# Optimization experiments

Measured on AMD Instinct MI355X. Metric: run time of the kernel, lower is better.

Reference implementation:

```python
import jax, jax.numpy as jnp
import numpy as np

N, N1, N2, K = 65536, 16384, 8192, 16
INDIM, HID, OUT = 64, 32, 128


def _knn_np(pos, q, k, chunk=1024):
    # brute-force chunked KNN (indices into pos) for setup only
    out = []
    for s in range(0, q.shape[0], chunk):
        d = ((q[s:s + chunk, None, :] - pos[None, :, :]) ** 2).sum(-1)
        out.append(np.argpartition(d, k, axis=1)[:, :k])
    return np.concatenate(out, 0)


def setup_inputs() -> dict:
    key = jax.random.key(0)
    ks = jax.random.split(key, 12)
    x = jax.random.normal(ks[0], (N, INDIM), jnp.float32)
    pos = jax.random.uniform(ks[1], (N, 3), jnp.float32)

    pos_np = np.asarray(pos)
    rng = np.random.default_rng(0)
    idx1 = np.sort(rng.choice(N, N1, replace=False))            # RandomSampler(ratio1)
    nn1 = _knn_np(pos_np, pos_np[idx1], K)                      # [N1, K] into full cloud
    src1, dst1 = nn1.reshape(-1), np.repeat(np.arange(N1), K)
    pos1 = pos_np[idx1]
    idx2 = np.sort(rng.choice(N1, N2, replace=False))           # RandomSampler(ratio2)
    nn2 = _knn_np(pos1, pos1[idx2], K)                          # [N2, K] into level-1 cloud
    src2, dst2 = nn2.reshape(-1), np.repeat(np.arange(N2), K)

    def lin(k, i, o):
        return jax.random.normal(k, (i, o), jnp.float32) / float(np.sqrt(i))

    return dict(
        x=x, pos=pos,
        W_down=lin(ks[2], INDIM, HID), b_down=jnp.zeros((HID,), jnp.float32),
        W_pp1=lin(ks[3], 10, 32), b_pp1=jnp.zeros((32,), jnp.float32),
        W_att1=lin(ks[4], 64, 64), b_att1=jnp.zeros((64,), jnp.float32),
        W_g1=lin(ks[5], 64, 64), b_g1=jnp.zeros((64,), jnp.float32),
        W_pp2=lin(ks[6], 10, 64), b_pp2=jnp.zeros((64,), jnp.float32),
        W_att2=lin(ks[7], 128, 128), b_att2=jnp.zeros((128,), jnp.float32),
        W_g2=lin(ks[8], 128, 128), b_g2=jnp.zeros((128,), jnp.float32),
        W_up=lin(ks[9], 128, OUT), b_up=jnp.zeros((OUT,), jnp.float32),
        W_sc=lin(ks[10], INDIM, OUT), b_sc=jnp.zeros((OUT,), jnp.float32),
        idx1=jnp.asarray(idx1, jnp.int32), idx2=jnp.asarray(idx2, jnp.int32),
        src1=jnp.asarray(src1, jnp.int32), dst1=jnp.asarray(dst1, jnp.int32),
        src2=jnp.asarray(src2, jnp.int32), dst2=jnp.asarray(dst2, jnp.int32),
    )


def _mlp(h, W, b):
    return jax.nn.relu(h @ W + b)


def _randla_conv(x, pos_all, pos_q, src, dst, Wpp, bpp, Watt, batt, Wg, bg, n_out):
    # RandlaKernel.message + add-aggregate + update (bipartite: targets = sampled points)
    pos_i, pos_j = pos_q[dst], pos_all[src]                     # [E,3]
    vij = pos_i - pos_j
    dij = jnp.sqrt((vij * vij).sum(-1, keepdims=True))          # [E,1]
    rel = jnp.concatenate([pos_i, pos_j, vij, dij], axis=1)     # [E,10]
    rij = _mlp(rel, Wpp, bpp)                                   # point_pos_nn
    fij = jnp.concatenate([x[src], rij], axis=1)                # [E, c+d]
    s = jax.nn.softmax(_mlp(fij, Watt, batt), axis=-1)          # softmax over feature dim (as in source)
    agg = jax.ops.segment_sum(s * fij, dst, num_segments=n_out) # aggr='add'
    return _mlp(agg, Wg, bg)                                    # global_nn


def reference(x, pos, W_down, b_down, W_pp1, b_pp1, W_att1, b_att1, W_g1, b_g1,
              W_pp2, b_pp2, W_att2, b_att2, W_g2, b_g2, W_up, b_up, W_sc, b_sc,
              idx1, idx2, src1, dst1, src2, dst2):
    h = _mlp(x, W_down, b_down)                                 # features_downsample (indim -> outdim//4)
    pos1 = pos[idx1]
    h = _randla_conv(h, pos, pos1, src1, dst1, W_pp1, b_pp1, W_att1, b_att1, W_g1, b_g1, N1)
    pos2 = pos1[idx2]
    h = _randla_conv(h, pos1, pos2, src2, dst2, W_pp2, b_pp2, W_att2, b_att2, W_g2, b_g2, N2)
    h = _mlp(h, W_up, b_up)                                     # features_upsample
    sc = _mlp(x[idx1][idx2], W_sc, b_sc)                        # shortcut resized, idx = idx1[idx2]
    return jax.nn.relu(h + sc)
```

## Files before the change

### kernel.cpp

```cpp
#include <hip/hip_runtime.h>

#define N_FULL 65536
#define NN1    16384
#define NN2    8192

typedef __attribute__((ext_vector_type(8))) short bf16x8;
typedef __attribute__((ext_vector_type(4))) float f32x4;
typedef unsigned short ushortT;

#define MFMA16(acc, a, b) acc = __builtin_amdgcn_mfma_f32_16x16x32_bf16(a, b, acc, 0, 0, 0)

static __device__ __forceinline__ ushortT f2bf(float f) {
    union { float f; unsigned u; } v; v.f = f;
    unsigned r = v.u + 0x7FFFu + ((v.u >> 16) & 1u);
    return (ushortT)(r >> 16);
}
static __device__ __forceinline__ unsigned pack2(float a, float b) {
    return (unsigned)f2bf(a) | ((unsigned)f2bf(b) << 16);
}
static __device__ __forceinline__ float bfu2f(ushortT h) {
    union { unsigned u; float f; } v; v.u = (unsigned)h << 16; return v.f;
}

#define WS_WDT   0
#define WS_WAT1  2304
#define WS_WGT1  6912
#define WS_WAT2  11520
#define WS_WGT2  28928
#define WS_WUPT  46336
#define WS_WSCT  63744
#define WS_H0    73728
#define WS_H1    (WS_H0 + 65536u*32u)
#define WS_AGG2  (WS_H1 + 16384u*64u)

static __device__ __forceinline__ void tpose(
    const float* __restrict__ src, ushortT* __restrict__ dst,
    int K, int N, int STR, int gid, int gs)
{
    for (int i = gid; i < K * N; i += gs) {
        const int n = i / K, k = i - n * K;
        dst[n * STR + k] = f2bf(src[(size_t)k * N + n]);
    }
}

__global__ __launch_bounds__(256) void k_prep(
    const float* __restrict__ Wd, const float* __restrict__ Wa1,
    const float* __restrict__ Wg1, const float* __restrict__ Wa2,
    const float* __restrict__ Wg2, const float* __restrict__ Wup,
    const float* __restrict__ Wsc, ushortT* __restrict__ wsw)
{
    const int gid = blockIdx.x * 256 + threadIdx.x, gs = gridDim.x * 256;
    tpose(Wd,  wsw + WS_WDT,  64, 32, 72,  gid, gs);
    tpose(Wa1, wsw + WS_WAT1, 64, 64, 72,  gid, gs);
    tpose(Wg1, wsw + WS_WGT1, 64, 64, 72,  gid, gs);
    tpose(Wa2, wsw + WS_WAT2, 128, 128, 136, gid, gs);
    tpose(Wg2, wsw + WS_WGT2, 128, 128, 136, gid, gs);
    tpose(Wup, wsw + WS_WUPT, 128, 128, 136, gid, gs);
    tpose(Wsc, wsw + WS_WSCT, 64, 128, 72, gid, gs);
}

__global__ __launch_bounds__(256) void k_down(
    const float* __restrict__ x, const ushortT* __restrict__ wsw,
    const float* __restrict__ bd, ushortT* __restrict__ h0w)
{
    __shared__ __align__(16) ushortT Al[128 * 72];
    __shared__ __align__(16) ushortT Bl[32 * 72];
    const int t = threadIdx.x;
    const int rowBase = blockIdx.x * 128;

    {
        const int r = t >> 1, c0 = (t & 1) * 32;
        unsigned* dst = (unsigned*)Al + r * 36 + (c0 >> 1);
        const float* src = &x[(size_t)(rowBase + r) * 64 + c0];
#pragma unroll
        for (int j = 0; j < 32; j += 4) {
            const float4 v = *reinterpret_cast<const float4*>(src + j);
            dst[(j >> 1) + 0] = pack2(v.x, v.y);
            dst[(j >> 1) + 1] = pack2(v.z, v.w);
        }
        const uint4* wsrc = (const uint4*)(wsw + WS_WDT);
        uint4* bl4 = (uint4*)Bl;
        for (int i = t; i < 288; i += 256) bl4[i] = wsrc[i];
    }
    __syncthreads();

    const int lane = t & 63, w = t >> 6, quad = lane >> 4, c16 = lane & 15;
    f32x4 acc[2][2];
#pragma unroll
    for (int mt = 0; mt < 2; ++mt)
#pragma unroll
        for (int nt = 0; nt < 2; ++nt)
#pragma unroll
            for (int r = 0; r < 4; ++r) acc[mt][nt][r] = 0.f;
#pragma unroll
    for (int ks = 0; ks < 2; ++ks) {
        bf16x8 a[2], b[2];
#pragma unroll
        for (int mt = 0; mt < 2; ++mt)
            a[mt] = *(const bf16x8*)&Al[(w * 32 + mt * 16 + c16) * 72 + ks * 32 + quad * 8];
#pragma unroll
        for (int nt = 0; nt < 2; ++nt)
            b[nt] = *(const bf16x8*)&Bl[(nt * 16 + c16) * 72 + ks * 32 + quad * 8];
#pragma unroll
        for (int mt = 0; mt < 2; ++mt)
#pragma unroll
            for (int nt = 0; nt < 2; ++nt) MFMA16(acc[mt][nt], a[mt], b[nt]);
    }
#pragma unroll
    for (int nt = 0; nt < 2; ++nt) {
        const int col = nt * 16 + c16;
        const float bias = bd[col];
#pragma unroll
        for (int mt = 0; mt < 2; ++mt)
#pragma unroll
            for (int r = 0; r < 4; ++r) {
                const int row = rowBase + w * 32 + mt * 16 + quad * 4 + r;
                h0w[(size_t)row * 32 + col] = f2bf(fmaxf(acc[mt][nt][r] + bias, 0.f));
            }
    }
}

__global__ __launch_bounds__(256) void k_conv1(
    const ushortT* __restrict__ h0w, const float* __restrict__ pos,
    const int* __restrict__ idx1, const int* __restrict__ src1,
    const float* __restrict__ Wpp, const float* __restrict__ bpp,
    const ushortT* __restrict__ wsw, const float* __restrict__ batt,
    const float* __restrict__ bg, ushortT* __restrict__ h1w)
{
    __shared__ __align__(16) ushortT Fl[128 * 72];
    __shared__ __align__(16) ushortT Wl[64 * 72];
    __shared__ __align__(16) ushortT Gl[64 * 72];
    __shared__ __align__(16) ushortT A2ls[16 * 72];
    __shared__ float Pl[352];
    const int t = threadIdx.x;
    const int d0 = blockIdx.x * 8;

    {
        const uint4* wa = (const uint4*)(wsw + WS_WAT1);
        const uint4* wg = (const uint4*)(wsw + WS_WGT1);
        uint4* wl4 = (uint4*)Wl;
        uint4* gl4 = (uint4*)Gl;
        for (int i = t; i < 576; i += 256) { wl4[i] = wa[i]; gl4[i] = wg[i]; }
        for (int i = t; i < 352; i += 256) Pl[i] = (i < 320) ? Wpp[i] : bpp[i - 320];
        for (int i = t; i < 288; i += 256) ((unsigned*)A2ls)[288 + i] = 0;
    }

    {
        const int e = t >> 1, half = t & 1;
        const int g = e >> 4;
        const int s = src1[(d0 + g) * 16 + (e & 15)];
        const uint4* srcp = (const uint4*)((const unsigned*)h0w + (size_t)s * 16 + half * 8);
        uint4* dstp = (uint4*)((unsigned*)Fl + e * 36 + half * 8);
        dstp[0] = srcp[0];
        dstp[1] = srcp[1];

        const int pin = idx1[d0 + g];
        const float pix = pos[pin * 3 + 0], piy = pos[pin * 3 + 1], piz = pos[pin * 3 + 2];
        const float pjx = pos[s * 3 + 0],  pjy = pos[s * 3 + 1],  pjz = pos[s * 3 + 2];
        const float vx = pix - pjx, vy = piy - pjy, vz = piz - pjz;
        const float dij = sqrtf(vx * vx + vy * vy + vz * vz);
        const float rel[10] = {pix, piy, piz, pjx, pjy, pjz, vx, vy, vz, dij};
        __syncthreads();
        const int c0 = half * 16;
#pragma unroll
        for (int c = 0; c < 16; c += 2) {
            float a0 = Pl[320 + c0 + c], a1 = Pl[320 + c0 + c + 1];
#pragma unroll
            for (int i = 0; i < 10; ++i) {
                a0 += rel[i] * Pl[i * 32 + c0 + c];
                a1 += rel[i] * Pl[i * 32 + c0 + c + 1];
            }
            ((unsigned*)Fl)[(e * 72 + 32 + c0 + c) >> 1] = pack2(fmaxf(a0, 0.f), fmaxf(a1, 0.f));
        }
    }
    __syncthreads();

    const int lane = t & 63, w = t >> 6, quad = lane >> 4, c16 = lane & 15;
    f32x4 acc[2][4];
#pragma unroll
    for (int mt = 0; mt < 2; ++mt)
#pragma unroll
        for (int nt = 0; nt < 4; ++nt)
#pragma unroll
            for (int r = 0; r < 4; ++r) acc[mt][nt][r] = 0.f;
#pragma unroll
    for (int ks = 0; ks < 2; ++ks) {
        bf16x8 a[2], b[4];
#pragma unroll
        for (int mt = 0; mt < 2; ++mt)
            a[mt] = *(const bf16x8*)&Fl[(w * 32 + mt * 16 + c16) * 72 + ks * 32 + quad * 8];
#pragma unroll
        for (int nt = 0; nt < 4; ++nt)
            b[nt] = *(const bf16x8*)&Wl[(nt * 16 + c16) * 72 + ks * 32 + quad * 8];
#pragma unroll
        for (int mt = 0; mt < 2; ++mt)
#pragma unroll
            for (int nt = 0; nt < 4; ++nt) MFMA16(acc[mt][nt], a[mt], b[nt]);
    }
    float bcol[4];
#pragma unroll
    for (int nt = 0; nt < 4; ++nt) bcol[nt] = batt[nt * 16 + c16];

#pragma unroll
    for (int mt = 0; mt < 2; ++mt) {
#pragma unroll
        for (int nt = 0; nt < 4; ++nt)
#pragma unroll
            for (int r = 0; r < 4; ++r)
                acc[mt][nt][r] = fmaxf(acc[mt][nt][r] + bcol[nt], 0.f);
        float rs[4];
#pragma unroll
        for (int r = 0; r < 4; ++r) {
            float mx = acc[mt][0][r];
#pragma unroll
            for (int nt = 1; nt < 4; ++nt) mx = fmaxf(mx, acc[mt][nt][r]);
            mx = fmaxf(mx, __shfl_xor(mx, 1));
            mx = fmaxf(mx, __shfl_xor(mx, 2));
            mx = fmaxf(mx, __shfl_xor(mx, 4));
            mx = fmaxf(mx, __shfl_xor(mx, 8));
            float sm = 0.f;
#pragma unroll
            for (int nt = 0; nt < 4; ++nt) {
                acc[mt][nt][r] = __expf(acc[mt][nt][r] - mx);
                sm += acc[mt][nt][r];
            }
            sm += __shfl_xor(sm, 1);
            sm += __shfl_xor(sm, 2);
            sm += __shfl_xor(sm, 4);
            sm += __shfl_xor(sm, 8);
            rs[r] = 1.f / sm;
        }
#pragma unroll
        for (int nt = 0; nt < 4; ++nt) {
            float v = 0.f;
#pragma unroll
            for (int r = 0; r < 4; ++r) {
                const float fv = bfu2f(Fl[(w * 32 + mt * 16 + quad * 4 + r) * 72 + nt * 16 + c16]);
                v += acc[mt][nt][r] * rs[r] * fv;
            }
            v += __shfl_xor(v, 16);
            v += __shfl_xor(v, 32);
            if (lane < 16)
                A2ls[(w * 2 + mt) * 72 + nt * 16 + c16] = f2bf(v);
        }
    }
    __syncthreads();

    {
        f32x4 acc2 = {0.f, 0.f, 0.f, 0.f};
#pragma unroll
        for (int ks = 0; ks < 2; ++ks) {
            const bf16x8 a = *(const bf16x8*)&A2ls[c16 * 72 + ks * 32 + quad * 8];
            const bf16x8 b = *(const bf16x8*)&Gl[(w * 16 + c16) * 72 + ks * 32 + quad * 8];
            MFMA16(acc2, a, b);
        }
        const int col = w * 16 + c16;
        const float bias = bg[col];
        if (quad < 2) {
#pragma unroll
            for (int r = 0; r < 4; ++r) {
                const int row = quad * 4 + r;
                h1w[(size_t)(d0 + row) * 64 + col] = f2bf(fmaxf(acc2[r] + bias, 0.f));
            }
        }
    }
}

__global__ __launch_bounds__(256) void k_conv2(
    const ushortT* __restrict__ h1w, const float* __restrict__ pos,
    const int* __restrict__ idx1, const int* __restrict__ idx2,
    const int* __restrict__ src2,
    const float* __restrict__ Wpp, const float* __restrict__ bpp,
    const ushortT* __restrict__ wsw, const float* __restrict__ batt,
    ushortT* __restrict__ agg2w)
{
    __shared__ __align__(16) ushortT Fl[128 * 136];
    __shared__ __align__(16) ushortT Wl[128 * 136];
    __shared__ float Pl[704];
    const int t = threadIdx.x;
    const int d0 = blockIdx.x * 8;

    {
        const uint4* wsrc = (const uint4*)(wsw + WS_WAT2);
        uint4* wl4 = (uint4*)Wl;
        for (int i = t; i < 2176; i += 256) wl4[i] = wsrc[i];
        for (int i = t; i < 704; i += 256) Pl[i] = (i < 640) ? Wpp[i] : bpp[i - 640];
    }

    {
        const int e = t >> 1, half = t & 1;
        const int g = e >> 4;
        const int s = src2[(d0 + g) * 16 + (e & 15)];
        const uint4* srcp = (const uint4*)((const unsigned*)h1w + (size_t)s * 32 + half * 16);
        uint4* dstp = (uint4*)((unsigned*)Fl + e * 68 + half * 16);
#pragma unroll
        for (int j = 0; j < 4; ++j) dstp[j] = srcp[j];

        const int pin = idx1[idx2[d0 + g]];
        const int sn = idx1[s];
        const float pix = pos[pin * 3 + 0], piy = pos[pin * 3 + 1], piz = pos[pin * 3 + 2];
        const float pjx = pos[sn * 3 + 0],  pjy = pos[sn * 3 + 1],  pjz = pos[sn * 3 + 2];
        const float vx = pix - pjx, vy = piy - pjy, vz = piz - pjz;
        const float dij = sqrtf(vx * vx + vy * vy + vz * vz);
        const float rel[10] = {pix, piy, piz, pjx, pjy, pjz, vx, vy, vz, dij};
        __syncthreads();
        const int c0 = half * 32;
#pragma unroll
        for (int c = 0; c < 32; c += 2) {
            float a0 = Pl[640 + c0 + c], a1 = Pl[640 + c0 + c + 1];
#pragma unroll
            for (int i = 0; i < 10; ++i) {
                a0 += rel[i] * Pl[i * 64 + c0 + c];
                a1 += rel[i] * Pl[i * 64 + c0 + c + 1];
            }
            ((unsigned*)Fl)[(e * 136 + 64 + c0 + c) >> 1] = pack2(fmaxf(a0, 0.f), fmaxf(a1, 0.f));
        }
    }
    __syncthreads();

    const int lane = t & 63, w = t >> 6, quad = lane >> 4, c16 = lane & 15;
    f32x4 acc[2][8];
#pragma unroll
    for (int mt = 0; mt < 2; ++mt)
#pragma unroll
        for (int nt = 0; nt < 8; ++nt)
#pragma unroll
            for (int r = 0; r < 4; ++r) acc[mt][nt][r] = 0.f;
#pragma unroll
    for (int ks = 0; ks < 4; ++ks) {
        bf16x8 a[2], b[8];
#pragma unroll
        for (int mt = 0; mt < 2; ++mt)
            a[mt] = *(const bf16x8*)&Fl[(w * 32 + mt * 16 + c16) * 136 + ks * 32 + quad * 8];
#pragma unroll
        for (int nt = 0; nt < 8; ++nt)
            b[nt] = *(const bf16x8*)&Wl[(nt * 16 + c16) * 136 + ks * 32 + quad * 8];
#pragma unroll
        for (int mt = 0; mt < 2; ++mt)
#pragma unroll
            for (int nt = 0; nt < 8; ++nt) MFMA16(acc[mt][nt], a[mt], b[nt]);
    }
    float bcol[8];
#pragma unroll
    for (int nt = 0; nt < 8; ++nt) bcol[nt] = batt[nt * 16 + c16];

#pragma unroll
    for (int mt = 0; mt < 2; ++mt) {
#pragma unroll
        for (int nt = 0; nt < 8; ++nt)
#pragma unroll
            for (int r = 0; r < 4; ++r)
                acc[mt][nt][r] = fmaxf(acc[mt][nt][r] + bcol[nt], 0.f);
        float rs[4];
#pragma unroll
        for (int r = 0; r < 4; ++r) {
            float mx = acc[mt][0][r];
#pragma unroll
            for (int nt = 1; nt < 8; ++nt) mx = fmaxf(mx, acc[mt][nt][r]);
            mx = fmaxf(mx, __shfl_xor(mx, 1));
            mx = fmaxf(mx, __shfl_xor(mx, 2));
            mx = fmaxf(mx, __shfl_xor(mx, 4));
            mx = fmaxf(mx, __shfl_xor(mx, 8));
            float sm = 0.f;
#pragma unroll
            for (int nt = 0; nt < 8; ++nt) {
                acc[mt][nt][r] = __expf(acc[mt][nt][r] - mx);
                sm += acc[mt][nt][r];
            }
            sm += __shfl_xor(sm, 1);
            sm += __shfl_xor(sm, 2);
            sm += __shfl_xor(sm, 4);
            sm += __shfl_xor(sm, 8);
            rs[r] = 1.f / sm;
        }
#pragma unroll
        for (int nt = 0; nt < 8; ++nt) {
            float v = 0.f;
#pragma unroll
            for (int r = 0; r < 4; ++r) {
                const float fv = bfu2f(Fl[(w * 32 + mt * 16 + quad * 4 + r) * 136 + nt * 16 + c16]);
                v += acc[mt][nt][r] * rs[r] * fv;
            }
            v += __shfl_xor(v, 16);
            v += __shfl_xor(v, 32);
            if (lane < 16)
                agg2w[(size_t)(d0 + w * 2 + mt) * 128 + nt * 16 + c16] = f2bf(v);
        }
    }
}

__global__ __launch_bounds__(256) void k_post(
    const ushortT* __restrict__ agg2w, const float* __restrict__ x,
    const int* __restrict__ idx1, const int* __restrict__ idx2,
    const ushortT* __restrict__ wsw,
    const float* __restrict__ bg, const float* __restrict__ bup,
    const float* __restrict__ bsc, float* __restrict__ out)
{
    __shared__ __align__(16) ushortT Al[32 * 136];
    __shared__ __align__(16) ushortT Wl[128 * 136];
    __shared__ __align__(16) ushortT Bl[32 * 136];
    __shared__ __align__(16) ushortT A2[32 * 72];
    const int t = threadIdx.x;
    const int d0 = blockIdx.x * 32;

    for (int i = t; i < 512; i += 256) {
        const int r = i >> 4, j = i & 15;
        ((uint4*)((unsigned*)Al + r * 68))[j] =
            ((const uint4*)((const unsigned*)agg2w + (size_t)(d0 + r) * 64))[j];
    }
    {
        const int r = t >> 3, q = t & 7;
        const int pin = idx1[idx2[d0 + r]];
        const float* src = &x[(size_t)pin * 64 + q * 8];
        unsigned* dst = (unsigned*)A2 + r * 36 + q * 4;
#pragma unroll
        for (int j = 0; j < 4; ++j) {
            const float2 v = *reinterpret_cast<const float2*>(src + j * 2);
            dst[j] = pack2(v.x, v.y);
        }
    }
    {
        const uint4* wsrc = (const uint4*)(wsw + WS_WGT2);
        uint4* wl4 = (uint4*)Wl;
        for (int i = t; i < 2176; i += 256) wl4[i] = wsrc[i];
    }
    __syncthreads();

    const int lane = t & 63, w = t >> 6, quad = lane >> 4, c16 = lane & 15;
    const int mtw = w >> 1;
    const int ntb = (w & 1) * 4;

    {
        f32x4 acc[4];
#pragma unroll
        for (int nt = 0; nt < 4; ++nt)
#pragma unroll
            for (int r = 0; r < 4; ++r) acc[nt][r] = 0.f;
#pragma unroll
        for (int ks = 0; ks < 4; ++ks) {
            const bf16x8 a = *(const bf16x8*)&Al[(mtw * 16 + c16) * 136 + ks * 32 + quad * 8];
#pragma unroll
            for (int nt = 0; nt < 4; ++nt) {
                const bf16x8 b = *(const bf16x8*)&Wl[((ntb + nt) * 16 + c16) * 136 + ks * 32 + quad * 8];
                MFMA16(acc[nt], a, b);
            }
        }
#pragma unroll
        for (int nt = 0; nt < 4; ++nt) {
            const int col = (ntb + nt) * 16 + c16;
            const float bias = bg[col];
#pragma unroll
            for (int r = 0; r < 4; ++r)
                Bl[(mtw * 16 + quad * 4 + r) * 136 + col] = f2bf(fmaxf(acc[nt][r] + bias, 0.f));
        }
    }
    __syncthreads();
    {
        const uint4* wsrc = (const uint4*)(wsw + WS_WUPT);
        uint4* wl4 = (uint4*)Wl;
        for (int i = t; i < 2176; i += 256) wl4[i] = wsrc[i];
    }
    __syncthreads();

    f32x4 u[4];
    {
#pragma unroll
        for (int nt = 0; nt < 4; ++nt)
#pragma unroll
            for (int r = 0; r < 4; ++r) u[nt][r] = 0.f;
#pragma unroll
        for (int ks = 0; ks < 4; ++ks) {
            const bf16x8 a = *(const bf16x8*)&Bl[(mtw * 16 + c16) * 136 + ks * 32 + quad * 8];
#pragma unroll
            for (int nt = 0; nt < 4; ++nt) {
                const bf16x8 b = *(const bf16x8*)&Wl[((ntb + nt) * 16 + c16) * 136 + ks * 32 + quad * 8];
                MFMA16(u[nt], a, b);
            }
        }
#pragma unroll
        for (int nt = 0; nt < 4; ++nt) {
            const float bias = bup[(ntb + nt) * 16 + c16];
#pragma unroll
            for (int r = 0; r < 4; ++r) u[nt][r] = fmaxf(u[nt][r] + bias, 0.f);
        }
    }
    __syncthreads();
    {
        const uint4* wsrc = (const uint4*)(wsw + WS_WSCT);
        uint4* wl4 = (uint4*)Wl;
        for (int i = t; i < 1152; i += 256) wl4[i] = wsrc[i];
    }
    __syncthreads();

    {
        f32x4 acc[4];
#pragma unroll
        for (int nt = 0; nt < 4; ++nt)
#pragma unroll
            for (int r = 0; r < 4; ++r) acc[nt][r] = 0.f;
#pragma unroll
        for (int ks = 0; ks < 2; ++ks) {
            const bf16x8 a = *(const bf16x8*)&A2[(mtw * 16 + c16) * 72 + ks * 32 + quad * 8];
#pragma unroll
            for (int nt = 0; nt < 4; ++nt) {
                const bf16x8 b = *(const bf16x8*)&Wl[((ntb + nt) * 16 + c16) * 72 + ks * 32 + quad * 8];
                MFMA16(acc[nt], a, b);
            }
        }
#pragma unroll
        for (int nt = 0; nt < 4; ++nt) {
            const int col = (ntb + nt) * 16 + c16;
            const float bias = bsc[col];
#pragma unroll
            for (int r = 0; r < 4; ++r) {
                const float sc = fmaxf(acc[nt][r] + bias, 0.f);
                const int row = d0 + mtw * 16 + quad * 4 + r;
                out[(size_t)row * 128 + col] = u[nt][r] + sc;
            }
        }
    }
}

extern "C" void kernel_launch(void* const* d_in, const int* in_sizes, int n_in,
                              void* d_out, int out_size, void* d_ws, size_t ws_size,
                              hipStream_t stream)
{
    const float* x      = (const float*)d_in[0];
    const float* pos    = (const float*)d_in[1];
    const float* W_down = (const float*)d_in[2];
    const float* b_down = (const float*)d_in[3];
    const float* W_pp1  = (const float*)d_in[4];
    const float* b_pp1  = (const float*)d_in[5];
    const float* W_att1 = (const float*)d_in[6];
    const float* b_att1 = (const float*)d_in[7];
    const float* W_g1   = (const float*)d_in[8];
    const float* b_g1   = (const float*)d_in[9];
    const float* W_pp2  = (const float*)d_in[10];
    const float* b_pp2  = (const float*)d_in[11];
    const float* W_att2 = (const float*)d_in[12];
    const float* b_att2 = (const float*)d_in[13];
    const float* W_g2   = (const float*)d_in[14];
    const float* b_g2   = (const float*)d_in[15];
    const float* W_up   = (const float*)d_in[16];
    const float* b_up   = (const float*)d_in[17];
    const float* W_sc   = (const float*)d_in[18];
    const float* b_sc   = (const float*)d_in[19];
    const int* idx1 = (const int*)d_in[20];
    const int* idx2 = (const int*)d_in[21];
    const int* src1 = (const int*)d_in[22];
    const int* src2 = (const int*)d_in[24];

    ushortT* wsw = (ushortT*)d_ws;
    ushortT* h0w   = wsw + WS_H0;
    ushortT* h1w   = wsw + WS_H1;
    ushortT* agg2w = wsw + WS_AGG2;

    k_prep <<<68, 256, 0, stream>>>(W_down, W_att1, W_g1, W_att2, W_g2, W_up, W_sc, wsw);
    k_down <<<N_FULL / 128, 256, 0, stream>>>(x, wsw, b_down, h0w);
    k_conv1<<<NN1 / 8, 256, 0, stream>>>(h0w, pos, idx1, src1,
                                         W_pp1, b_pp1, wsw, b_att1, b_g1, h1w);
    k_conv2<<<NN2 / 8, 256, 0, stream>>>(h1w, pos, idx1, idx2, src2,
                                         W_pp2, b_pp2, wsw, b_att2, agg2w);
    k_post <<<NN2 / 32, 256, 0, stream>>>(agg2w, x, idx1, idx2, wsw,
                                          b_g2, b_up, b_sc, (float*)d_out);
}
```

Before: 183.4 us.

## Fuse weight prep into downsample kernel and read MFMA weights from global

Merges the weight-transpose prep kernel into k_down as extra blocks, and k_down now transposes W_down itself from the fp32 source, which removes one launch. The conv and post kernels drop their LDS staging of the transposed weights and load B fragments directly from the global workspace. This also removes several __syncthreads and the LDS footprint, which may raise occupancy. It also switches to the hardware packed bf16 conversion when available. The cost is repeated, uncoalesced global/L2 reads of weight fragments inside the MFMA loops.

```diff
diff --git a/kernel.cpp b/kernel.cpp
--- a/kernel.cpp
+++ b/kernel.cpp
@@ -10,6 +10,19 @@
 
 #define MFMA16(acc, a, b) acc = __builtin_amdgcn_mfma_f32_16x16x32_bf16(a, b, acc, 0, 0, 0)
 
+#if __has_builtin(__builtin_amdgcn_cvt_pk_bf16_f32)
+typedef __attribute__((ext_vector_type(2))) __bf16 bf16x2t;
+static __device__ __forceinline__ unsigned pack2(float a, float b) {
+    union { bf16x2t v; unsigned u; } c;
+    c.v = __builtin_amdgcn_cvt_pk_bf16_f32(a, b);
+    return c.u;
+}
+static __device__ __forceinline__ ushortT f2bf(float f) {
+    union { bf16x2t v; ushortT s[2]; } c;
+    c.v = __builtin_amdgcn_cvt_pk_bf16_f32(f, 0.f);
+    return c.s[0];
+}
+#else
 static __device__ __forceinline__ ushortT f2bf(float f) {
     union { float f; unsigned u; } v; v.f = f;
     unsigned r = v.u + 0x7FFFu + ((v.u >> 16) & 1u);
@@ -18,11 +31,12 @@
 static __device__ __forceinline__ unsigned pack2(float a, float b) {
     return (unsigned)f2bf(a) | ((unsigned)f2bf(b) << 16);
 }
+#endif
+
 static __device__ __forceinline__ float bfu2f(ushortT h) {
     union { unsigned u; float f; } v; v.u = (unsigned)h << 16; return v.f;
 }
 
-#define WS_WDT   0
 #define WS_WAT1  2304
 #define WS_WGT1  6912
 #define WS_WAT2  11520
@@ -43,29 +57,28 @@
     }
 }
 
-__global__ __launch_bounds__(256) void k_prep(
-    const float* __restrict__ Wd, const float* __restrict__ Wa1,
-    const float* __restrict__ Wg1, const float* __restrict__ Wa2,
-    const float* __restrict__ Wg2, const float* __restrict__ Wup,
-    const float* __restrict__ Wsc, ushortT* __restrict__ wsw)
+__global__ __launch_bounds__(256) void k_down(
+    const float* __restrict__ x, const float* __restrict__ Wd,
+    const float* __restrict__ bd,
+    const float* __restrict__ Wa1, const float* __restrict__ Wg1,
+    const float* __restrict__ Wa2, const float* __restrict__ Wg2,
+    const float* __restrict__ Wup, const float* __restrict__ Wsc,
+    ushortT* __restrict__ wsw, ushortT* __restrict__ h0w)
 {
-    const int gid = blockIdx.x * 256 + threadIdx.x, gs = gridDim.x * 256;
-    tpose(Wd,  wsw + WS_WDT,  64, 32, 72,  gid, gs);
-    tpose(Wa1, wsw + WS_WAT1, 64, 64, 72,  gid, gs);
-    tpose(Wg1, wsw + WS_WGT1, 64, 64, 72,  gid, gs);
-    tpose(Wa2, wsw + WS_WAT2, 128, 128, 136, gid, gs);
-    tpose(Wg2, wsw + WS_WGT2, 128, 128, 136, gid, gs);
-    tpose(Wup, wsw + WS_WUPT, 128, 128, 136, gid, gs);
-    tpose(Wsc, wsw + WS_WSCT, 64, 128, 72, gid, gs);
-}
-
-__global__ __launch_bounds__(256) void k_down(
-    const float* __restrict__ x, const ushortT* __restrict__ wsw,
-    const float* __restrict__ bd, ushortT* __restrict__ h0w)
-{
+    const int t = threadIdx.x;
+    if (blockIdx.x >= 512) {
+        const int gid = (blockIdx.x - 512) * 256 + t, gs = 68 * 256;
+        tpose(Wa1, wsw + WS_WAT1, 64, 64, 72, gid, gs);
+        tpose(Wg1, wsw + WS_WGT1, 64, 64, 72, gid, gs);
+        tpose(Wa2, wsw + WS_WAT2, 128, 128, 136, gid, gs);
+        tpose(Wg2, wsw + WS_WGT2, 128, 128, 136, gid, gs);
+        tpose(Wup, wsw + WS_WUPT, 128, 128, 136, gid, gs);
+        tpose(Wsc, wsw + WS_WSCT, 64, 128, 72, gid, gs);
+        return;
+    }
+
     __shared__ __align__(16) ushortT Al[128 * 72];
     __shared__ __align__(16) ushortT Bl[32 * 72];
-    const int t = threadIdx.x;
     const int rowBase = blockIdx.x * 128;
 
     {
@@ -78,9 +91,14 @@
             dst[(j >> 1) + 0] = pack2(v.x, v.y);
             dst[(j >> 1) + 1] = pack2(v.z, v.w);
         }
-        const uint4* wsrc = (const uint4*)(wsw + WS_WDT);
-        uint4* bl4 = (uint4*)Bl;
-        for (int i = t; i < 288; i += 256) bl4[i] = wsrc[i];
+        const int n = t >> 3, kc = (t & 7) * 8;
+        float v[8];
+#pragma unroll
+        for (int j = 0; j < 8; ++j) v[j] = Wd[(size_t)(kc + j) * 32 + n];
+        uint4 p;
+        p.x = pack2(v[0], v[1]); p.y = pack2(v[2], v[3]);
+        p.z = pack2(v[4], v[5]); p.w = pack2(v[6], v[7]);
+        *(uint4*)((unsigned*)Bl + n * 36 + (kc >> 1)) = p;
     }
     __syncthreads();
 
@@ -128,22 +146,13 @@
     const float* __restrict__ bg, ushortT* __restrict__ h1w)
 {
     __shared__ __align__(16) ushortT Fl[128 * 72];
-    __shared__ __align__(16) ushortT Wl[64 * 72];
-    __shared__ __align__(16) ushortT Gl[64 * 72];
     __shared__ __align__(16) ushortT A2ls[16 * 72];
     __shared__ float Pl[352];
     const int t = threadIdx.x;
     const int d0 = blockIdx.x * 8;
 
-    {
-        const uint4* wa = (const uint4*)(wsw + WS_WAT1);
-        const uint4* wg = (const uint4*)(wsw + WS_WGT1);
-        uint4* wl4 = (uint4*)Wl;
-        uint4* gl4 = (uint4*)Gl;
-        for (int i = t; i < 576; i += 256) { wl4[i] = wa[i]; gl4[i] = wg[i]; }
-        for (int i = t; i < 352; i += 256) Pl[i] = (i < 320) ? Wpp[i] : bpp[i - 320];
-        for (int i = t; i < 288; i += 256) ((unsigned*)A2ls)[288 + i] = 0;
-    }
+    for (int i = t; i < 352; i += 256) Pl[i] = (i < 320) ? Wpp[i] : bpp[i - 320];
+    for (int i = t; i < 288; i += 256) ((unsigned*)A2ls)[288 + i] = 0;
 
     {
         const int e = t >> 1, half = t & 1;
@@ -176,6 +185,7 @@
     __syncthreads();
 
     const int lane = t & 63, w = t >> 6, quad = lane >> 4, c16 = lane & 15;
+    const ushortT* WB = wsw + WS_WAT1;
     f32x4 acc[2][4];
 #pragma unroll
     for (int mt = 0; mt < 2; ++mt)
@@ -185,17 +195,16 @@
             for (int r = 0; r < 4; ++r) acc[mt][nt][r] = 0.f;
 #pragma unroll
     for (int ks = 0; ks < 2; ++ks) {
-        bf16x8 a[2], b[4];
+        bf16x8 a[2];
 #pragma unroll
         for (int mt = 0; mt < 2; ++mt)
             a[mt] = *(const bf16x8*)&Fl[(w * 32 + mt * 16 + c16) * 72 + ks * 32 + quad * 8];
 #pragma unroll
-        for (int nt = 0; nt < 4; ++nt)
-            b[nt] = *(const bf16x8*)&Wl[(nt * 16 + c16) * 72 + ks * 32 + quad * 8];
-#pragma unroll
-        for (int mt = 0; mt < 2; ++mt)
-#pragma unroll
-            for (int nt = 0; nt < 4; ++nt) MFMA16(acc[mt][nt], a[mt], b[nt]);
+        for (int nt = 0; nt < 4; ++nt) {
+            const bf16x8 b = *(const bf16x8*)&WB[(nt * 16 + c16) * 72 + ks * 32 + quad * 8];
+#pragma unroll
+            for (int mt = 0; mt < 2; ++mt) MFMA16(acc[mt][nt], a[mt], b);
+        }
     }
     float bcol[4];
 #pragma unroll
@@ -247,11 +256,12 @@
     __syncthreads();
 
     {
+        const ushortT* GB = wsw + WS_WGT1;
         f32x4 acc2 = {0.f, 0.f, 0.f, 0.f};
 #pragma unroll
         for (int ks = 0; ks < 2; ++ks) {
             const bf16x8 a = *(const bf16x8*)&A2ls[c16 * 72 + ks * 32 + quad * 8];
-            const bf16x8 b = *(const bf16x8*)&Gl[(w * 16 + c16) * 72 + ks * 32 + quad * 8];
+            const bf16x8 b = *(const bf16x8*)&GB[(w * 16 + c16) * 72 + ks * 32 + quad * 8];
             MFMA16(acc2, a, b);
         }
         const int col = w * 16 + c16;
@@ -275,17 +285,11 @@
     ushortT* __restrict__ agg2w)
 {
     __shared__ __align__(16) ushortT Fl[128 * 136];
-    __shared__ __align__(16) ushortT Wl[128 * 136];
     __shared__ float Pl[704];
     const int t = threadIdx.x;
     const int d0 = blockIdx.x * 8;
 
-    {
-        const uint4* wsrc = (const uint4*)(wsw + WS_WAT2);
-        uint4* wl4 = (uint4*)Wl;
-        for (int i = t; i < 2176; i += 256) wl4[i] = wsrc[i];
-        for (int i = t; i < 704; i += 256) Pl[i] = (i < 640) ? Wpp[i] : bpp[i - 640];
-    }
+    for (int i = t; i < 704; i += 256) Pl[i] = (i < 640) ? Wpp[i] : bpp[i - 640];
 
     {
         const int e = t >> 1, half = t & 1;
@@ -319,6 +323,7 @@
     __syncthreads();
 
     const int lane = t & 63, w = t >> 6, quad = lane >> 4, c16 = lane & 15;
+    const ushortT* WB = wsw + WS_WAT2;
     f32x4 acc[2][8];
 #pragma unroll
     for (int mt = 0; mt < 2; ++mt)
@@ -328,17 +333,16 @@
             for (int r = 0; r < 4; ++r) acc[mt][nt][r] = 0.f;
 #pragma unroll
     for (int ks = 0; ks < 4; ++ks) {
-        bf16x8 a[2], b[8];
+        bf16x8 a[2];
 #pragma unroll
         for (int mt = 0; mt < 2; ++mt)
             a[mt] = *(const bf16x8*)&Fl[(w * 32 + mt * 16 + c16) * 136 + ks * 32 + quad * 8];
 #pragma unroll
-        for (int nt = 0; nt < 8; ++nt)
-            b[nt] = *(const bf16x8*)&Wl[(nt * 16 + c16) * 136 + ks * 32 + quad * 8];
-#pragma unroll
-        for (int mt = 0; mt < 2; ++mt)
-#pragma unroll
-            for (int nt = 0; nt < 8; ++nt) MFMA16(acc[mt][nt], a[mt], b[nt]);
+        for (int nt = 0; nt < 8; ++nt) {
+            const bf16x8 b = *(const bf16x8*)&WB[(nt * 16 + c16) * 136 + ks * 32 + quad * 8];
+#pragma unroll
+            for (int mt = 0; mt < 2; ++mt) MFMA16(acc[mt][nt], a[mt], b);
+        }
     }
     float bcol[8];
 #pragma unroll
@@ -397,7 +401,6 @@
     const float* __restrict__ bsc, float* __restrict__ out)
 {
     __shared__ __align__(16) ushortT Al[32 * 136];
-    __shared__ __align__(16) ushortT Wl[128 * 136];
     __shared__ __align__(16) ushortT Bl[32 * 136];
     __shared__ __align__(16) ushortT A2[32 * 72];
     const int t = threadIdx.x;
@@ -419,11 +422,6 @@
             dst[j] = pack2(v.x, v.y);
         }
     }
-    {
-        const uint4* wsrc = (const uint4*)(wsw + WS_WGT2);
-        uint4* wl4 = (uint4*)Wl;
-        for (int i = t; i < 2176; i += 256) wl4[i] = wsrc[i];
-    }
     __syncthreads();
 
     const int lane = t & 63, w = t >> 6, quad = lane >> 4, c16 = lane & 15;
@@ -431,6 +429,7 @@
     const int ntb = (w & 1) * 4;
 
     {
+        const ushortT* WB = wsw + WS_WGT2;
         f32x4 acc[4];
 #pragma unroll
         for (int nt = 0; nt < 4; ++nt)
@@ -441,7 +440,7 @@
             const bf16x8 a = *(const bf16x8*)&Al[(mtw * 16 + c16) * 136 + ks * 32 + quad * 8];
 #pragma unroll
             for (int nt = 0; nt < 4; ++nt) {
-                const bf16x8 b = *(const bf16x8*)&Wl[((ntb + nt) * 16 + c16) * 136 + ks * 32 + quad * 8];
+                const bf16x8 b = *(const bf16x8*)&WB[((ntb + nt) * 16 + c16) * 136 + ks * 32 + quad * 8];
                 MFMA16(acc[nt], a, b);
             }
         }
@@ -455,15 +454,10 @@
         }
     }
     __syncthreads();
-    {
-        const uint4* wsrc = (const uint4*)(wsw + WS_WUPT);
-        uint4* wl4 = (uint4*)Wl;
-        for (int i = t; i < 2176; i += 256) wl4[i] = wsrc[i];
-    }
-    __syncthreads();
 
     f32x4 u[4];
     {
+        const ushortT* WB = wsw + WS_WUPT;
 #pragma unroll
         for (int nt = 0; nt < 4; ++nt)
 #pragma unroll
@@ -473,7 +467,7 @@
             const bf16x8 a = *(const bf16x8*)&Bl[(mtw * 16 + c16) * 136 + ks * 32 + quad * 8];
 #pragma unroll
             for (int nt = 0; nt < 4; ++nt) {
-                const bf16x8 b = *(const bf16x8*)&Wl[((ntb + nt) * 16 + c16) * 136 + ks * 32 + quad * 8];
+                const bf16x8 b = *(const bf16x8*)&WB[((ntb + nt) * 16 + c16) * 136 + ks * 32 + quad * 8];
                 MFMA16(u[nt], a, b);
             }
         }
@@ -484,15 +478,9 @@
             for (int r = 0; r < 4; ++r) u[nt][r] = fmaxf(u[nt][r] + bias, 0.f);
         }
     }
-    __syncthreads();
-    {
-        const uint4* wsrc = (const uint4*)(wsw + WS_WSCT);
-        uint4* wl4 = (uint4*)Wl;
-        for (int i = t; i < 1152; i += 256) wl4[i] = wsrc[i];
-    }
-    __syncthreads();
-
-    {
+
+    {
+        const ushortT* WB = wsw + WS_WSCT;
         f32x4 acc[4];
 #pragma unroll
         for (int nt = 0; nt < 4; ++nt)
@@ -503,7 +491,7 @@
             const bf16x8 a = *(const bf16x8*)&A2[(mtw * 16 + c16) * 72 + ks * 32 + quad * 8];
 #pragma unroll
             for (int nt = 0; nt < 4; ++nt) {
-                const bf16x8 b = *(const bf16x8*)&Wl[((ntb + nt) * 16 + c16) * 72 + ks * 32 + quad * 8];
+                const bf16x8 b = *(const bf16x8*)&WB[((ntb + nt) * 16 + c16) * 72 + ks * 32 + quad * 8];
                 MFMA16(acc[nt], a, b);
             }
         }
@@ -555,8 +543,9 @@
     ushortT* h1w   = wsw + WS_H1;
     ushortT* agg2w = wsw + WS_AGG2;
 
-    k_prep <<<68, 256, 0, stream>>>(W_down, W_att1, W_g1, W_att2, W_g2, W_up, W_sc, wsw);
-    k_down <<<N_FULL / 128, 256, 0, stream>>>(x, wsw, b_down, h0w);
+    k_down <<<512 + 68, 256, 0, stream>>>(x, W_down, b_down,
+                                          W_att1, W_g1, W_att2, W_g2, W_up, W_sc,
+                                          wsw, h0w);
     k_conv1<<<NN1 / 8, 256, 0, stream>>>(h0w, pos, idx1, src1,
                                          W_pp1, b_pp1, wsw, b_att1, b_g1, h1w);
     k_conv2<<<NN2 / 8, 256, 0, stream>>>(h1w, pos, idx1, idx2, src2,
```

New measurement: 180.5 us. Within noise of the previous version (-1.6%).
